# Kernel tuning notes

Hardware: AMD Instinct MI355X
Metric: run time of the kernel (lower is better)

Reference implementation:

```python
import jax, jax.numpy as jnp
import numpy as np

B, N, F, H = 8, 4096, 128, 3  # graphs, nodes (max_types), embedding_size, nhid
ALPHA = 0.2                    # leaky-relu slope from StateNetwork's GAT(..., 0.2, ...)
NEG_INF = -9e15                # masked-softmax fill used by standard GraphAttentionLayer


def setup_inputs() -> dict:
    key = jax.random.key(0)
    ks = jax.random.split(key, 6)
    adj = jax.random.randint(ks[0], (B, N, N), 0, 2, dtype=jnp.int32)
    emb = jax.random.normal(ks[1], (N, F), dtype=jnp.float32)            # state_ent_emb.weight
    W = jax.random.normal(ks[2], (F, H), dtype=jnp.float32) * 0.1        # GAT layer weight
    a = jax.random.normal(ks[3], (2 * H, 1), dtype=jnp.float32) * 0.1    # GAT attention vector
    fc1_w = jax.random.normal(ks[4], (100, N * H), dtype=jnp.float32) * 0.01
    fc1_b = jnp.zeros((100,), dtype=jnp.float32)
    return {"adj": adj, "emb": emb, "W": W, "a": a, "fc1_w": fc1_w, "fc1_b": fc1_b}


def reference(adj, emb, W, a, fc1_w, fc1_b):
    # GAT input x = state_ent_emb.weight is SHARED across graphs, so Wh and the
    # unmasked pairwise scores e are computed once; only the adjacency mask varies.
    Wh = emb @ W                                   # [N, H]
    e_src = Wh @ a[:H]                             # [N, 1]
    e_dst = Wh @ a[H:]                             # [N, 1]
    e = jax.nn.leaky_relu(e_src + e_dst.T, negative_slope=ALPHA)  # [N, N]
    masked = jnp.where(adj > 0, e[None, :, :], NEG_INF)           # [B, N, N]
    attn = jax.nn.softmax(masked, axis=-1)                        # [B, N, N]
    h = jnp.einsum('bij,jh->bih', attn, Wh)                       # [B, N, H]
    h = jax.nn.elu(h)                              # concat=True head -> elu
    out = h.reshape(h.shape[0], -1)                # [B, N*H], per-graph flatten
    return out @ fc1_w.T + fc1_b                   # [B, 100]
```

## Files before the change

### kernel.cpp

```cpp
#include <hip/hip_runtime.h>
#include <hip/hip_bf16.h>
#include <math.h>

#define NNODES 4096
#define FDIM 128
#define HDIM 3
#define BGRAPH 8
#define GAT_ALPHA 0.2f

typedef int v4i __attribute__((ext_vector_type(4)));

__global__ __launch_bounds__(256) void wh_kernel(
    const float* __restrict__ emb, const float* __restrict__ W,
    const float* __restrict__ a,
    float4* __restrict__ tbl, float* __restrict__ esrc) {
    int wid = threadIdx.x >> 6, lane = threadIdx.x & 63;
    int i = blockIdx.x * 4 + wid;
    const float2 ev = *reinterpret_cast<const float2*>(emb + (size_t)i * FDIM + lane * 2);
    int t0 = lane * 2;
    float wh0 = ev.x * W[t0 * 3 + 0] + ev.y * W[(t0 + 1) * 3 + 0];
    float wh1 = ev.x * W[t0 * 3 + 1] + ev.y * W[(t0 + 1) * 3 + 1];
    float wh2 = ev.x * W[t0 * 3 + 2] + ev.y * W[(t0 + 1) * 3 + 2];
    for (int off = 32; off >= 1; off >>= 1) {
        wh0 += __shfl_xor(wh0, off);
        wh1 += __shfl_xor(wh1, off);
        wh2 += __shfl_xor(wh2, off);
    }
    if (lane == 0) {
        float es = wh0 * a[0] + wh1 * a[1] + wh2 * a[2];
        float ed = wh0 * a[3] + wh1 * a[4] + wh2 * a[5];
        tbl[i] = make_float4(wh0, wh1, wh2, ed);
        esrc[i] = es;
    }
}

__global__ __launch_bounds__(512, 4) void attn_kernel(
    const int* __restrict__ adj, const float4* __restrict__ tbl,
    const float* __restrict__ esrc, float* __restrict__ hout) {
    __shared__ float4 ltbl[NNODES];
    __shared__ float4 red[8];
    int tid = threadIdx.x;
    int wid = tid >> 6, lane = tid & 63;

    float s0 = 0.f, s1 = 0.f, s2 = 0.f, mx = -INFINITY;
    for (int k = tid; k < NNODES; k += 512) {
        float4 v = tbl[k];
        ltbl[(k & 3) * 1024 + (k >> 2)] = v;
        s0 += v.x; s1 += v.y; s2 += v.z; mx = fmaxf(mx, v.w);
    }
    for (int off = 32; off >= 1; off >>= 1) {
        s0 += __shfl_xor(s0, off);
        s1 += __shfl_xor(s1, off);
        s2 += __shfl_xor(s2, off);
        mx = fmaxf(mx, __shfl_xor(mx, off));
    }
    if (lane == 0) red[wid] = make_float4(s0, s1, s2, mx);
    __syncthreads();
    if (tid < 8) {
        float4 v = red[tid];
        for (int off = 4; off >= 1; off >>= 1) {
            v.x += __shfl_xor(v.x, off);
            v.y += __shfl_xor(v.y, off);
            v.z += __shfl_xor(v.z, off);
            v.w = fmaxf(v.w, __shfl_xor(v.w, off));
        }
        if (tid == 0) red[0] = v;
    }
    __syncthreads();
    const float4 st = red[0];
    const float L2E = 1.4426950408889634f;

    int i = blockIdx.x * 8 + wid;
    float es = esrc[i];
    float m = es + st.w;
    m = fmaxf(m, GAT_ALPHA * m);
    float bias = -m * L2E;

    const v4i* ap[BGRAPH];
    #pragma unroll
    for (int g = 0; g < BGRAPH; ++g)
        ap[g] = reinterpret_cast<const v4i*>(adj + ((size_t)g * NNODES + i) * NNODES);

    float sw[BGRAPH], a0[BGRAPH], a1[BGRAPH], a2[BGRAPH];
    #pragma unroll
    for (int g = 0; g < BGRAPH; ++g) { sw[g] = 0.f; a0[g] = 0.f; a1[g] = 0.f; a2[g] = 0.f; }

    #pragma unroll 1
    for (int T = 0; T < 16; ++T) {
        int base = T * 64 + lane;
        v4i av[BGRAPH];
        #pragma unroll
        for (int g = 0; g < BGRAPH; ++g)
            av[g] = __builtin_nontemporal_load(ap[g] + base);
        #pragma unroll
        for (int c = 0; c < 4; ++c) {
            float4 tv = ltbl[c * 1024 + base];
            float t = es + tv.w;
            float x = fmaxf(t, GAT_ALPHA * t);
            float w = __builtin_amdgcn_exp2f(x * L2E + bias);
            #pragma unroll
            for (int g = 0; g < BGRAPH; ++g) {
                float wg = (av[g][c] > 0) ? w : 0.f;
                sw[g] += wg;
                a0[g] += wg * tv.x;
                a1[g] += wg * tv.y;
                a2[g] += wg * tv.z;
            }
        }
    }

    #pragma unroll
    for (int g = 0; g < BGRAPH; ++g) {
        for (int off = 32; off >= 1; off >>= 1) {
            sw[g] += __shfl_xor(sw[g], off);
            a0[g] += __shfl_xor(a0[g], off);
            a1[g] += __shfl_xor(a1[g], off);
            a2[g] += __shfl_xor(a2[g], off);
        }
    }
    if (lane == 0) {
        #pragma unroll
        for (int g = 0; g < BGRAPH; ++g) {
            float h0, h1, h2;
            if (sw[g] > 0.f) {
                h0 = a0[g] / sw[g]; h1 = a1[g] / sw[g]; h2 = a2[g] / sw[g];
            } else {
                h0 = st.x * (1.f / NNODES);
                h1 = st.y * (1.f / NNODES);
                h2 = st.z * (1.f / NNODES);
            }
            h0 = h0 > 0.f ? h0 : expf(h0) - 1.f;
            h1 = h1 > 0.f ? h1 : expf(h1) - 1.f;
            h2 = h2 > 0.f ? h2 : expf(h2) - 1.f;
            float* hp = hout + ((size_t)g * NNODES + i) * 3;
            hp[0] = h0; hp[1] = h1; hp[2] = h2;
        }
    }
}

__global__ void fc_kernel(const float* __restrict__ h, const float* __restrict__ w,
                          const float* __restrict__ bias, float* __restrict__ out) {
    int bo = blockIdx.x;
    int bg = bo / 100, o = bo % 100;
    const float* hrow = h + (size_t)bg * (NNODES * HDIM);
    const float* wrow = w + (size_t)o * (NNODES * HDIM);
    int tid = threadIdx.x;
    float p = 0.f;
    for (int k = tid; k < NNODES * HDIM; k += 256) p += hrow[k] * wrow[k];
    __shared__ float sh[256];
    sh[tid] = p;
    __syncthreads();
    for (int off = 128; off >= 1; off >>= 1) {
        if (tid < off) sh[tid] += sh[tid + off];
        __syncthreads();
    }
    if (tid == 0) out[bo] = sh[0] + bias[o];
}

extern "C" void kernel_launch(void* const* d_in, const int* in_sizes, int n_in,
                              void* d_out, int out_size, void* d_ws, size_t ws_size,
                              hipStream_t stream) {
    const int*   adj  = (const int*)d_in[0];
    const float* emb  = (const float*)d_in[1];
    const float* W    = (const float*)d_in[2];
    const float* a    = (const float*)d_in[3];
    const float* fc1w = (const float*)d_in[4];
    const float* fc1b = (const float*)d_in[5];
    float* out = (float*)d_out;

    char* ws = (char*)d_ws;
    float4* tbl  = (float4*)ws;
    float*  esrc = (float*)(ws + 65536);
    float*  hout = (float*)(ws + 65536 + 16384);

    wh_kernel<<<NNODES / 4, 256, 0, stream>>>(emb, W, a, tbl, esrc);
    attn_kernel<<<512, 512, 0, stream>>>(adj, tbl, esrc, hout);
    fc_kernel<<<BGRAPH * 100, 256, 0, stream>>>(hout, fc1w, fc1b, out);
}
```

Before: 128.1 us.

## Process graphs in pairs to cut register pressure; vectorize fc dot product

The attention kernel now loops over the 8 graphs two at a time, keeping 8 accumulators live instead of 32 and issuing two adjacency loads per iteration instead of eight. This lowers register pressure and may allow more waves per SIMD. The cost is recomputing the exp weights and re-reading the LDS table four times, and having fewer loads in flight per wave. Separately, the fc kernel switches to float4 loads with a fully unrolled loop.

```diff
diff --git a/kernel.cpp b/kernel.cpp
--- a/kernel.cpp
+++ b/kernel.cpp
@@ -75,78 +75,77 @@
     float m = es + st.w;
     m = fmaxf(m, GAT_ALPHA * m);
     float bias = -m * L2E;
-
-    const v4i* ap[BGRAPH];
-    #pragma unroll
-    for (int g = 0; g < BGRAPH; ++g)
-        ap[g] = reinterpret_cast<const v4i*>(adj + ((size_t)g * NNODES + i) * NNODES);
-
-    float sw[BGRAPH], a0[BGRAPH], a1[BGRAPH], a2[BGRAPH];
-    #pragma unroll
-    for (int g = 0; g < BGRAPH; ++g) { sw[g] = 0.f; a0[g] = 0.f; a1[g] = 0.f; a2[g] = 0.f; }
+    const size_t GSTRIDE = (size_t)NNODES * NNODES / 4;
 
     #pragma unroll 1
-    for (int T = 0; T < 16; ++T) {
-        int base = T * 64 + lane;
-        v4i av[BGRAPH];
-        #pragma unroll
-        for (int g = 0; g < BGRAPH; ++g)
-            av[g] = __builtin_nontemporal_load(ap[g] + base);
-        #pragma unroll
-        for (int c = 0; c < 4; ++c) {
-            float4 tv = ltbl[c * 1024 + base];
-            float t = es + tv.w;
-            float x = fmaxf(t, GAT_ALPHA * t);
-            float w = __builtin_amdgcn_exp2f(x * L2E + bias);
+    for (int p = 0; p < 4; ++p) {
+        const v4i* ap0 = reinterpret_cast<const v4i*>(adj + ((size_t)(2 * p) * NNODES + i) * NNODES);
+        const v4i* ap1 = ap0 + GSTRIDE;
+
+        float sA = 0.f, xA = 0.f, yA = 0.f, zA = 0.f;
+        float sB = 0.f, xB = 0.f, yB = 0.f, zB = 0.f;
+        #pragma unroll 2
+        for (int T = 0; T < 16; ++T) {
+            int base = T * 64 + lane;
+            v4i av0 = __builtin_nontemporal_load(ap0 + base);
+            v4i av1 = __builtin_nontemporal_load(ap1 + base);
             #pragma unroll
-            for (int g = 0; g < BGRAPH; ++g) {
-                float wg = (av[g][c] > 0) ? w : 0.f;
-                sw[g] += wg;
-                a0[g] += wg * tv.x;
-                a1[g] += wg * tv.y;
-                a2[g] += wg * tv.z;
+            for (int c = 0; c < 4; ++c) {
+                float4 tv = ltbl[c * 1024 + base];
+                float t = es + tv.w;
+                float x = fmaxf(t, GAT_ALPHA * t);
+                float w = __builtin_amdgcn_exp2f(x * L2E + bias);
+                float w0 = (av0[c] > 0) ? w : 0.f;
+                float w1 = (av1[c] > 0) ? w : 0.f;
+                sA += w0; xA += w0 * tv.x; yA += w0 * tv.y; zA += w0 * tv.z;
+                sB += w1; xB += w1 * tv.x; yB += w1 * tv.y; zB += w1 * tv.z;
             }
         }
-    }
-
-    #pragma unroll
-    for (int g = 0; g < BGRAPH; ++g) {
         for (int off = 32; off >= 1; off >>= 1) {
-            sw[g] += __shfl_xor(sw[g], off);
-            a0[g] += __shfl_xor(a0[g], off);
-            a1[g] += __shfl_xor(a1[g], off);
-            a2[g] += __shfl_xor(a2[g], off);
+            sA += __shfl_xor(sA, off); xA += __shfl_xor(xA, off);
+            yA += __shfl_xor(yA, off); zA += __shfl_xor(zA, off);
+            sB += __shfl_xor(sB, off); xB += __shfl_xor(xB, off);
+            yB += __shfl_xor(yB, off); zB += __shfl_xor(zB, off);
         }
-    }
-    if (lane == 0) {
-        #pragma unroll
-        for (int g = 0; g < BGRAPH; ++g) {
-            float h0, h1, h2;
-            if (sw[g] > 0.f) {
-                h0 = a0[g] / sw[g]; h1 = a1[g] / sw[g]; h2 = a2[g] / sw[g];
-            } else {
-                h0 = st.x * (1.f / NNODES);
-                h1 = st.y * (1.f / NNODES);
-                h2 = st.z * (1.f / NNODES);
+        if (lane == 0) {
+            #pragma unroll
+            for (int q = 0; q < 2; ++q) {
+                float sw = q ? sB : sA;
+                float h0, h1, h2;
+                if (sw > 0.f) {
+                    h0 = (q ? xB : xA) / sw;
+                    h1 = (q ? yB : yA) / sw;
+                    h2 = (q ? zB : zA) / sw;
+                } else {
+                    h0 = st.x * (1.f / NNODES);
+                    h1 = st.y * (1.f / NNODES);
+                    h2 = st.z * (1.f / NNODES);
+                }
+                h0 = h0 > 0.f ? h0 : expf(h0) - 1.f;
+                h1 = h1 > 0.f ? h1 : expf(h1) - 1.f;
+                h2 = h2 > 0.f ? h2 : expf(h2) - 1.f;
+                float* hp = hout + ((size_t)(2 * p + q) * NNODES + i) * 3;
+                hp[0] = h0; hp[1] = h1; hp[2] = h2;
             }
-            h0 = h0 > 0.f ? h0 : expf(h0) - 1.f;
-            h1 = h1 > 0.f ? h1 : expf(h1) - 1.f;
-            h2 = h2 > 0.f ? h2 : expf(h2) - 1.f;
-            float* hp = hout + ((size_t)g * NNODES + i) * 3;
-            hp[0] = h0; hp[1] = h1; hp[2] = h2;
         }
     }
 }
 
-__global__ void fc_kernel(const float* __restrict__ h, const float* __restrict__ w,
-                          const float* __restrict__ bias, float* __restrict__ out) {
+__global__ __launch_bounds__(256) void fc_kernel(
+    const float* __restrict__ h, const float* __restrict__ w,
+    const float* __restrict__ bias, float* __restrict__ out) {
     int bo = blockIdx.x;
     int bg = bo / 100, o = bo % 100;
-    const float* hrow = h + (size_t)bg * (NNODES * HDIM);
-    const float* wrow = w + (size_t)o * (NNODES * HDIM);
+    const float4* hrow = reinterpret_cast<const float4*>(h + (size_t)bg * (NNODES * HDIM));
+    const float4* wrow = reinterpret_cast<const float4*>(w + (size_t)o * (NNODES * HDIM));
     int tid = threadIdx.x;
     float p = 0.f;
-    for (int k = tid; k < NNODES * HDIM; k += 256) p += hrow[k] * wrow[k];
+    #pragma unroll
+    for (int k = 0; k < 12; ++k) {
+        float4 hv = hrow[k * 256 + tid];
+        float4 wv = wrow[k * 256 + tid];
+        p += hv.x * wv.x + hv.y * wv.y + hv.z * wv.z + hv.w * wv.w;
+    }
     __shared__ float sh[256];
     sh[tid] = p;
     __syncthreads();
```

New measurement: 103.4 us, median of 2. 1.24x faster.
